# Optimization experiments

Measured on AMD Instinct MI355X. Metric: run time of the kernel, lower is better.

The kernel has to match this reference:

```python
import jax, jax.numpy as jnp
import numpy as np

B, T, N, E, H, MAXD = 32, 128, 42, 256, 8, 7
DH = E // H


def _hand_edges():
    left = [(0, 1), (1, 2), (2, 3), (3, 4), (0, 5), (5, 6), (6, 7), (7, 8), (0, 9), (9, 10), (10, 11), (11, 12), (0, 13), (13, 14), (14, 15), (15, 16), (0, 17), (17, 18), (18, 19), (19, 20)]
    right = [(21, 22), (22, 23), (23, 24), (24, 25), (21, 26), (26, 27), (27, 28), (28, 29), (21, 30), (30, 31), (31, 32), (32, 33), (21, 34), (34, 35), (35, 36), (36, 37), (21, 38), (38, 39), (39, 40), (40, 41)]
    tips = [(4, 8), (8, 12), (12, 16), (16, 20), (25, 29), (29, 33), (33, 37), (37, 41)]
    cross = [(0, 21)]
    return left + right + cross + tips


def _graph_constants():
    adj = np.zeros((N, N), dtype=np.float32)
    dist = np.zeros((N, N), dtype=np.float64)
    for a, b in _hand_edges():
        adj[a, b] = 1.0
        adj[b, a] = 1.0
        dist[a, b] = 1.0
        dist[b, a] = 1.0
    # exact replica of the module's single-pass Floyd-Warshall-style loop
    for k in range(N):
        for i in range(N):
            for j in range(N):
                if i != j and dist[i, k] > 0 and dist[k, j] > 0:
                    nd = dist[i, k] + dist[k, j]
                    if dist[i, j] == 0 or nd < dist[i, j]:
                        dist[i, j] = nd
    dist = np.clip(dist, 0, MAXD).astype(np.int32)
    return adj, dist


def setup_inputs() -> dict:
    key = jax.random.key(0)
    ks = jax.random.split(key, 12)
    adj_np, dist_np = _graph_constants()
    s_in = 1.0 / np.sqrt(E)
    return {
        'node_features': jax.random.normal(ks[0], (B, T, N, E), dtype=jnp.float32),
        'adjacency_matrix': jnp.asarray(adj_np),
        'distances': jnp.asarray(dist_np),
        'Wq': jax.random.normal(ks[1], (E, E), dtype=jnp.float32) * s_in,
        'bq': jnp.zeros((E,), dtype=jnp.float32),
        'Wk': jax.random.normal(ks[2], (E, E), dtype=jnp.float32) * s_in,
        'bk': jnp.zeros((E,), dtype=jnp.float32),
        'Wv': jax.random.normal(ks[3], (E, E), dtype=jnp.float32) * s_in,
        'bv': jnp.zeros((E,), dtype=jnp.float32),
        'Wo': jax.random.normal(ks[4], (E, E), dtype=jnp.float32) * s_in,
        'bo': jnp.zeros((E,), dtype=jnp.float32),
        'rel_emb': jax.random.normal(ks[5], (2 * MAXD + 1, H), dtype=jnp.float32) * 0.05,
    }


def reference(node_features, adjacency_matrix, distances, Wq, bq, Wk, bk, Wv, bv, Wo, bo, rel_emb):
    b, t, n, e = node_features.shape
    q = (node_features @ Wq + bq).reshape(b, t, n, H, DH)
    k = (node_features @ Wk + bk).reshape(b, t, n, H, DH)
    v = (node_features @ Wv + bv).reshape(b, t, n, H, DH)
    # scores: [b, t, h, i, j]
    scores = jnp.einsum('btihd,btjhd->bthij', q, k) / jnp.sqrt(jnp.float32(DH))
    # relative position bias: [n, n, h] -> [h, n, n]
    bias = rel_emb[distances]  # (N, N, H)
    scores = scores + jnp.transpose(bias, (2, 0, 1))[None, None]
    mask = (adjacency_matrix > 0).astype(jnp.float32)[None, None, None]
    scores = scores * mask + (1.0 - mask) * (-1e9)
    attn = jax.nn.softmax(scores, axis=-1)
    out = jnp.einsum('bthij,btjhd->btihd', attn, v).reshape(b, t, n, e)
    out = out @ Wo + bo
    return out, attn
```

## Files before the change

### kernel.cpp

```cpp
#include <hip/hip_runtime.h>
#include <stdint.h>


#define TPB 512
constexpr int BT = 4096;
constexpr int N = 42, NP = 48, E = 256, H = 8;
constexpr int NE = N * E;
constexpr int NN = N * N;
constexpr float SCALE = 0.17677669529663687f;

typedef short sh8 __attribute__((ext_vector_type(8)));
typedef float f4 __attribute__((ext_vector_type(4)));

__device__ __forceinline__ uint32_t cvtpk(float lo, float hi) {
  uint32_t d;
  asm("v_cvt_pk_bf16_f32 %0, %1, %2" : "=v"(d) : "v"(lo), "v"(hi));
  return d;
}
__device__ __forceinline__ uint16_t f2b1(float f) { return (uint16_t)cvtpk(f, f); }
__device__ __forceinline__ float b2f(uint16_t u) {
  union { uint32_t i; float f; } v; v.i = ((uint32_t)u) << 16; return v.f;
}

#define SWZ(base, row, cb) \
  ((char*)(base) + ((((row) << 9) + (cb)) ^ (((row) & 7) << 4)))

__global__ __launch_bounds__(256) void wt_kernel(
    const float* __restrict__ Wq, const float* __restrict__ Wk,
    const float* __restrict__ Wv, const float* __restrict__ Wo,
    uint16_t* __restrict__ WT) {
  __shared__ float tl[32][33];
  const int z = blockIdx.z;
  const float* W = (z == 0) ? Wq : (z == 1) ? Wk : (z == 2) ? Wv : Wo;
  uint16_t* dst = WT + z * 65536;
  const int k0 = blockIdx.y * 32, n0 = blockIdx.x * 32;
  const int r = threadIdx.x >> 5, cc = threadIdx.x & 31;
#pragma unroll
  for (int p = 0; p < 4; ++p)
    tl[r + 8 * p][cc] = W[(k0 + r + 8 * p) * E + n0 + cc];
  __syncthreads();
#pragma unroll
  for (int p = 0; p < 4; ++p)
    dst[(n0 + r + 8 * p) * E + k0 + cc] = f2b1(tl[cc][r + 8 * p]);
}

__device__ __forceinline__ void gemm_pass(const uint16_t* __restrict__ Wt,
                                          const char* Xb, int c, int lg, int nt0,
                                          f4 acc[3][2]) {
#pragma unroll
  for (int mt = 0; mt < 3; ++mt)
#pragma unroll
    for (int nt = 0; nt < 2; ++nt) acc[mt][nt] = (f4){0.f, 0.f, 0.f, 0.f};
  for (int kc = 0; kc < E; kc += 32) {
    sh8 xa[3];
#pragma unroll
    for (int mt = 0; mt < 3; ++mt)
      xa[mt] = *(const sh8*)SWZ(Xb, 16 * mt + c, (kc + 8 * lg) * 2);
#pragma unroll
    for (int nt = 0; nt < 2; ++nt) {
      const sh8 b8 = *(const sh8*)(Wt + ((nt0 + nt) * 16 + c) * E + kc + 8 * lg);
#pragma unroll
      for (int mt = 0; mt < 3; ++mt)
        acc[mt][nt] = __builtin_amdgcn_mfma_f32_16x16x32_bf16(xa[mt], b8, acc[mt][nt], 0, 0, 0);
    }
  }
}

__device__ __forceinline__ void tr_qk(const f4 acc[3][2], const float* __restrict__ bias,
                                      int n0, int c, int lg, uint16_t* scr, sh8 fr[3]) {
#pragma unroll
  for (int nt = 0; nt < 2; ++nt) {
    const float bv = bias[n0 + 16 * nt + c];
#pragma unroll
    for (int mt = 0; mt < 3; ++mt)
#pragma unroll
      for (int r = 0; r < 4; ++r)
        scr[(16 * mt + 4 * lg + r) * 40 + 16 * nt + c] = f2b1(acc[mt][nt][r] + bv);
  }
#pragma unroll
  for (int mt = 0; mt < 3; ++mt)
    fr[mt] = *(const sh8*)(scr + (16 * mt + c) * 40 + 8 * lg);
}

__global__ __launch_bounds__(TPB, 2) void gt_kernel(
    const float* __restrict__ X, const float* __restrict__ adj,
    const int* __restrict__ dist,
    const float* __restrict__ bq, const float* __restrict__ bk,
    const float* __restrict__ bv, const float* __restrict__ bo,
    const float* __restrict__ rel, const uint16_t* __restrict__ WT,
    float* __restrict__ out, float* __restrict__ attn) {
  alignas(16) __shared__ char smem[70368];
  char* const Xb = smem;
  uint16_t* const VT = (uint16_t*)smem;
  uint8_t*  const dm8 = (uint8_t*)(smem + 67584);
  float*    const relL = (float*)(smem + 69888);

  const int gid = blockIdx.x;
  const int tid = threadIdx.x;
  const int w = tid >> 6, lane = tid & 63, c = lane & 15, lg = lane >> 4;
  const int nt0 = 2 * w, n0 = 32 * w;
  uint16_t* const scr = (uint16_t*)(smem + 24576 + w * 5376);

  {
    const float4* Xs = (const float4*)(X + (size_t)gid * NE);
    for (int i = tid; i < NE / 4; i += TPB) {
      const float4 v = Xs[i];
      uint2 pk; pk.x = cvtpk(v.x, v.y); pk.y = cvtpk(v.z, v.w);
      *(uint2*)SWZ(Xb, i >> 6, (i & 63) << 3) = pk;
    }
    for (int i = tid; i < (NP - N) * 64; i += TPB) {
      uint2 z; z.x = 0u; z.y = 0u;
      *(uint2*)SWZ(Xb, N + (i >> 6), (i & 63) << 3) = z;
    }
    for (int t = tid; t < NP * NP; t += TPB) {
      const int i = t / NP, j = t - i * NP;
      uint8_t v = 0;
      if (i < N && j < N) {
        const float a = adj[i * N + j];
        v = (uint8_t)dist[i * N + j] | (a > 0.f ? 0x80 : 0);
      }
      dm8[t] = v;
    }
    for (int t = tid; t < 120; t += TPB) relL[t] = rel[t];
  }
  __syncthreads();

  sh8 qa[3], kb[3];
  {
    f4 acc[3][2];
    gemm_pass(WT, Xb, c, lg, nt0, acc);
    tr_qk(acc, bq, n0, c, lg, scr, qa);
    gemm_pass(WT + 65536, Xb, c, lg, nt0, acc);
    tr_qk(acc, bk, n0, c, lg, scr, kb);
  }
  f4 av[3][2];
  gemm_pass(WT + 131072, Xb, c, lg, nt0, av);
  __syncthreads();

#pragma unroll
  for (int nt = 0; nt < 2; ++nt) {
    const int n = n0 + 16 * nt + c;
    const float bvv = bv[n];
#pragma unroll
    for (int mt = 0; mt < 3; ++mt) {
      uint2 pk;
      pk.x = cvtpk(av[mt][nt][0] + bvv, av[mt][nt][1] + bvv);
      pk.y = cvtpk(av[mt][nt][2] + bvv, av[mt][nt][3] + bvv);
      *(uint2*)((char*)VT + n * 96 + 32 * mt + 8 * lg) = pk;
    }
  }

  {
    const int h = w;
    f4 st[3][3];
#pragma unroll
    for (int mt = 0; mt < 3; ++mt)
#pragma unroll
      for (int nt = 0; nt < 3; ++nt) {
        st[mt][nt] = (f4){0.f, 0.f, 0.f, 0.f};
        st[mt][nt] = __builtin_amdgcn_mfma_f32_16x16x32_bf16(kb[mt], qa[nt], st[mt][nt], 0, 0, 0);
      }

    uint16_t* const Psw = scr;
#pragma unroll
    for (int nt = 0; nt < 3; ++nt) {
      const int i = 16 * nt + c;
      float sv[12];
#pragma unroll
      for (int mt = 0; mt < 3; ++mt)
#pragma unroll
        for (int r = 0; r < 4; ++r) {
          const int j = 16 * mt + 4 * lg + r;
          const uint8_t dm = dm8[i * NP + j];
          const float s = st[mt][nt][r] * SCALE + relL[(dm & 0x7f) * 8 + h];
          sv[mt * 4 + r] = (dm & 0x80) ? s : -1e9f;
        }
      float m = sv[0];
#pragma unroll
      for (int k = 1; k < 12; ++k) m = fmaxf(m, sv[k]);
      m = fmaxf(m, __shfl_xor(m, 16));
      m = fmaxf(m, __shfl_xor(m, 32));
      float p[12], sum = 0.f;
#pragma unroll
      for (int k = 0; k < 12; ++k) { p[k] = __expf(sv[k] - m); sum += p[k]; }
      sum += __shfl_xor(sum, 16);
      sum += __shfl_xor(sum, 32);
      const float inv = __builtin_amdgcn_rcpf(sum);
#pragma unroll
      for (int mt = 0; mt < 3; ++mt) {
        const uint32_t d0 = cvtpk(p[mt * 4 + 0] * inv, p[mt * 4 + 1] * inv);
        const uint32_t d1 = cvtpk(p[mt * 4 + 2] * inv, p[mt * 4 + 3] * inv);
        char* base = (char*)Psw + i * 112 + 32 * mt + 8 * lg;
        *(uint32_t*)base = d0;
        *(uint32_t*)(base + 4) = d1;
      }
    }

    const sh8 z8 = {0, 0, 0, 0, 0, 0, 0, 0};
    sh8 pa0[3], pa1[3], vb0[2], vb1[2];
#pragma unroll
    for (int mt = 0; mt < 3; ++mt) {
      char* base = (char*)Psw + (16 * mt + c) * 112;
      pa0[mt] = *(const sh8*)(base + 16 * lg);
      pa1[mt] = (lg < 2) ? *(const sh8*)(base + 64 + 16 * lg) : z8;
    }
#pragma unroll
    for (int nt = 0; nt < 2; ++nt) {
      char* base = (char*)VT + (n0 + 16 * nt + c) * 96;
      vb0[nt] = *(const sh8*)(base + 16 * lg);
      vb1[nt] = (lg < 2) ? *(const sh8*)(base + 64 + 16 * lg) : z8;
    }
    f4 ov[3][2];
#pragma unroll
    for (int mt = 0; mt < 3; ++mt)
#pragma unroll
      for (int nt = 0; nt < 2; ++nt) {
        ov[mt][nt] = (f4){0.f, 0.f, 0.f, 0.f};
        ov[mt][nt] = __builtin_amdgcn_mfma_f32_16x16x32_bf16(pa0[mt], vb0[nt], ov[mt][nt], 0, 0, 0);
        ov[mt][nt] = __builtin_amdgcn_mfma_f32_16x16x32_bf16(pa1[mt], vb1[nt], ov[mt][nt], 0, 0, 0);
      }

    const size_t abase = ((size_t)gid * H + h) * (size_t)NN;
    for (int p = lane; p < NN; p += 64) {
      const int i = p / N, j = p - i * N;
      attn[abase + p] = b2f(Psw[i * 56 + j]);
    }
    __syncthreads();

#pragma unroll
    for (int mt = 0; mt < 3; ++mt)
#pragma unroll
      for (int nt = 0; nt < 2; ++nt)
#pragma unroll
        for (int r = 0; r < 4; ++r)
          *(uint16_t*)SWZ(Xb, 16 * mt + 4 * lg + r, (n0 + 16 * nt + c) * 2) =
              f2b1(ov[mt][nt][r]);
  }
  __syncthreads();

  {
    f4 ao[3][2];
    gemm_pass(WT + 196608, Xb, c, lg, nt0, ao);
#pragma unroll
    for (int nt = 0; nt < 2; ++nt) {
      const int n = n0 + 16 * nt + c;
      const float bov = bo[n];
#pragma unroll
      for (int mt = 0; mt < 3; ++mt)
#pragma unroll
        for (int r = 0; r < 4; ++r) {
          const int i = 16 * mt + 4 * lg + r;
          if (i < N) out[(size_t)gid * NE + i * E + n] = ao[mt][nt][r] + bov;
        }
    }
  }
}

extern "C" void kernel_launch(void* const* d_in, const int* in_sizes, int n_in,
                              void* d_out, int out_size, void* d_ws, size_t ws_size,
                              hipStream_t stream) {
  const float* X    = (const float*)d_in[0];
  const float* adj  = (const float*)d_in[1];
  const int*   dist = (const int*)d_in[2];
  const float* Wq   = (const float*)d_in[3];
  const float* bq   = (const float*)d_in[4];
  const float* Wk   = (const float*)d_in[5];
  const float* bk   = (const float*)d_in[6];
  const float* Wv   = (const float*)d_in[7];
  const float* bv   = (const float*)d_in[8];
  const float* Wo   = (const float*)d_in[9];
  const float* bo   = (const float*)d_in[10];
  const float* rel  = (const float*)d_in[11];
  float* out  = (float*)d_out;
  float* attn = out + (size_t)BT * NE;
  uint16_t* WT = (uint16_t*)d_ws;

  wt_kernel<<<dim3(8, 8, 4), dim3(256), 0, stream>>>(Wq, Wk, Wv, Wo, WT);
  gt_kernel<<<dim3(BT), dim3(TPB), 0, stream>>>(
      X, adj, dist, bq, bk, bv, bo, rel, WT, out, attn);
}
```

Before: 437.7 us.

## Split fused kernel into QKV projection and attention+output kernels via global scratch

Splits the single fused graph-transformer kernel into a QKV projection kernel and an attention plus Wo kernel. Q, K and transposed V are staged through workspace memory in bf16. The distance/adjacency byte table is precomputed once in the weight-transpose kernel. The aim is higher occupancy per kernel (launch bounds raised to 4 blocks) and shorter per-kernel register and LDS live ranges, at the cost of roughly 75 MB of extra global write and read traffic plus an extra launch.

```diff
diff --git a/kernel.cpp b/kernel.cpp
--- a/kernel.cpp
+++ b/kernel.cpp
@@ -9,6 +9,12 @@
 constexpr int NN = N * N;
 constexpr float SCALE = 0.17677669529663687f;
 
+constexpr size_t WT_OFF = 0;
+constexpr size_t DM_OFF = 524288;
+constexpr size_t Q_OFF  = 528384;
+constexpr size_t K_OFF  = Q_OFF + (size_t)BT * 48 * 256 * 2;
+constexpr size_t VT_OFF = K_OFF + (size_t)BT * 48 * 256 * 2;
+
 typedef short sh8 __attribute__((ext_vector_type(8)));
 typedef float f4 __attribute__((ext_vector_type(4)));
 
@@ -28,9 +34,22 @@
 __global__ __launch_bounds__(256) void wt_kernel(
     const float* __restrict__ Wq, const float* __restrict__ Wk,
     const float* __restrict__ Wv, const float* __restrict__ Wo,
-    uint16_t* __restrict__ WT) {
+    const float* __restrict__ adj, const int* __restrict__ dist,
+    uint16_t* __restrict__ WT, uint8_t* __restrict__ dm8g) {
+  const int z = blockIdx.z;
+  if (z == 4) {
+    if (blockIdx.x == 0 && blockIdx.y == 0) {
+      for (int t = threadIdx.x; t < NP * NP; t += 256) {
+        const int i = t / NP, j = t - i * NP;
+        uint8_t v = 0;
+        if (i < N && j < N)
+          v = (uint8_t)dist[i * N + j] | (adj[i * N + j] > 0.f ? 0x80 : 0);
+        dm8g[t] = v;
+      }
+    }
+    return;
+  }
   __shared__ float tl[32][33];
-  const int z = blockIdx.z;
   const float* W = (z == 0) ? Wq : (z == 1) ? Wk : (z == 2) ? Wv : Wo;
   uint16_t* dst = WT + z * 65536;
   const int k0 = blockIdx.y * 32, n0 = blockIdx.x * 32;
@@ -66,40 +85,17 @@
   }
 }
 
-__device__ __forceinline__ void tr_qk(const f4 acc[3][2], const float* __restrict__ bias,
-                                      int n0, int c, int lg, uint16_t* scr, sh8 fr[3]) {
-#pragma unroll
-  for (int nt = 0; nt < 2; ++nt) {
-    const float bv = bias[n0 + 16 * nt + c];
-#pragma unroll
-    for (int mt = 0; mt < 3; ++mt)
-#pragma unroll
-      for (int r = 0; r < 4; ++r)
-        scr[(16 * mt + 4 * lg + r) * 40 + 16 * nt + c] = f2b1(acc[mt][nt][r] + bv);
-  }
-#pragma unroll
-  for (int mt = 0; mt < 3; ++mt)
-    fr[mt] = *(const sh8*)(scr + (16 * mt + c) * 40 + 8 * lg);
-}
-
-__global__ __launch_bounds__(TPB, 2) void gt_kernel(
-    const float* __restrict__ X, const float* __restrict__ adj,
-    const int* __restrict__ dist,
+__global__ __launch_bounds__(TPB, 4) void qkv_kernel(
+    const float* __restrict__ X,
     const float* __restrict__ bq, const float* __restrict__ bk,
-    const float* __restrict__ bv, const float* __restrict__ bo,
-    const float* __restrict__ rel, const uint16_t* __restrict__ WT,
-    float* __restrict__ out, float* __restrict__ attn) {
-  alignas(16) __shared__ char smem[70368];
-  char* const Xb = smem;
-  uint16_t* const VT = (uint16_t*)smem;
-  uint8_t*  const dm8 = (uint8_t*)(smem + 67584);
-  float*    const relL = (float*)(smem + 69888);
-
+    const float* __restrict__ bv, const uint16_t* __restrict__ WT,
+    uint16_t* __restrict__ Qg, uint16_t* __restrict__ Kg,
+    char* __restrict__ VTg) {
+  alignas(16) __shared__ char Xb[NP * 512];
   const int gid = blockIdx.x;
   const int tid = threadIdx.x;
   const int w = tid >> 6, lane = tid & 63, c = lane & 15, lg = lane >> 4;
   const int nt0 = 2 * w, n0 = 32 * w;
-  uint16_t* const scr = (uint16_t*)(smem + 24576 + w * 5376);
 
   {
     const float4* Xs = (const float4*)(X + (size_t)gid * NE);
@@ -112,135 +108,170 @@
       uint2 z; z.x = 0u; z.y = 0u;
       *(uint2*)SWZ(Xb, N + (i >> 6), (i & 63) << 3) = z;
     }
-    for (int t = tid; t < NP * NP; t += TPB) {
-      const int i = t / NP, j = t - i * NP;
-      uint8_t v = 0;
-      if (i < N && j < N) {
-        const float a = adj[i * N + j];
-        v = (uint8_t)dist[i * N + j] | (a > 0.f ? 0x80 : 0);
-      }
-      dm8[t] = v;
-    }
-    for (int t = tid; t < 120; t += TPB) relL[t] = rel[t];
   }
   __syncthreads();
 
-  sh8 qa[3], kb[3];
-  {
-    f4 acc[3][2];
-    gemm_pass(WT, Xb, c, lg, nt0, acc);
-    tr_qk(acc, bq, n0, c, lg, scr, qa);
-    gemm_pass(WT + 65536, Xb, c, lg, nt0, acc);
-    tr_qk(acc, bk, n0, c, lg, scr, kb);
-  }
-  f4 av[3][2];
-  gemm_pass(WT + 131072, Xb, c, lg, nt0, av);
-  __syncthreads();
-
+  f4 acc[3][2];
+  gemm_pass(WT, Xb, c, lg, nt0, acc);
 #pragma unroll
   for (int nt = 0; nt < 2; ++nt) {
     const int n = n0 + 16 * nt + c;
-    const float bvv = bv[n];
+    const float bv_ = bq[n];
+#pragma unroll
+    for (int mt = 0; mt < 3; ++mt)
+#pragma unroll
+      for (int r = 0; r < 4; ++r) {
+        const int i = 16 * mt + 4 * lg + r;
+        Qg[((size_t)gid * 48 + i) * 256 + n] = f2b1(acc[mt][nt][r] + bv_);
+      }
+  }
+  gemm_pass(WT + 65536, Xb, c, lg, nt0, acc);
+#pragma unroll
+  for (int nt = 0; nt < 2; ++nt) {
+    const int n = n0 + 16 * nt + c;
+    const float bv_ = bk[n];
+#pragma unroll
+    for (int mt = 0; mt < 3; ++mt)
+#pragma unroll
+      for (int r = 0; r < 4; ++r) {
+        const int i = 16 * mt + 4 * lg + r;
+        Kg[((size_t)gid * 48 + i) * 256 + n] = f2b1(acc[mt][nt][r] + bv_);
+      }
+  }
+  gemm_pass(WT + 131072, Xb, c, lg, nt0, acc);
+  char* const vt = VTg + (size_t)gid * 24576;
+#pragma unroll
+  for (int nt = 0; nt < 2; ++nt) {
+    const int n = n0 + 16 * nt + c;
+    const float bv_ = bv[n];
 #pragma unroll
     for (int mt = 0; mt < 3; ++mt) {
       uint2 pk;
-      pk.x = cvtpk(av[mt][nt][0] + bvv, av[mt][nt][1] + bvv);
-      pk.y = cvtpk(av[mt][nt][2] + bvv, av[mt][nt][3] + bvv);
-      *(uint2*)((char*)VT + n * 96 + 32 * mt + 8 * lg) = pk;
+      pk.x = cvtpk(acc[mt][nt][0] + bv_, acc[mt][nt][1] + bv_);
+      pk.y = cvtpk(acc[mt][nt][2] + bv_, acc[mt][nt][3] + bv_);
+      *(uint2*)(vt + n * 96 + 32 * mt + 8 * lg) = pk;
+    }
+  }
+}
+
+__global__ __launch_bounds__(TPB, 4) void attn_wo_kernel(
+    const float* __restrict__ bo, const float* __restrict__ rel,
+    const uint16_t* __restrict__ WT, const uint16_t* __restrict__ Qg,
+    const uint16_t* __restrict__ Kg, const char* __restrict__ VTg,
+    const uint8_t* __restrict__ dm8g,
+    float* __restrict__ out, float* __restrict__ attn) {
+  alignas(16) __shared__ char smem[70368];
+  char* const Ob = smem;
+  uint8_t* const dm8 = (uint8_t*)(smem + 67584);
+  float*   const relL = (float*)(smem + 69888);
+
+  const int gid = blockIdx.x;
+  const int tid = threadIdx.x;
+  const int w = tid >> 6, lane = tid & 63, c = lane & 15, lg = lane >> 4;
+  const int nt0 = 2 * w, n0 = 32 * w, h = w;
+  uint16_t* const scr = (uint16_t*)(smem + 24576 + w * 5376);
+
+  for (int t = tid; t < NP * NP; t += TPB) dm8[t] = dm8g[t];
+  for (int t = tid; t < 120; t += TPB) relL[t] = rel[t];
+  __syncthreads();
+
+  sh8 qa[3], kb[3];
+#pragma unroll
+  for (int mt = 0; mt < 3; ++mt) {
+    const size_t ro = ((size_t)gid * 48 + 16 * mt + c) * 256 + 32 * h + 8 * lg;
+    qa[mt] = *(const sh8*)(Qg + ro);
+    kb[mt] = *(const sh8*)(Kg + ro);
+  }
+
+  f4 st[3][3];
+#pragma unroll
+  for (int mt = 0; mt < 3; ++mt)
+#pragma unroll
+    for (int nt = 0; nt < 3; ++nt) {
+      st[mt][nt] = (f4){0.f, 0.f, 0.f, 0.f};
+      st[mt][nt] = __builtin_amdgcn_mfma_f32_16x16x32_bf16(kb[mt], qa[nt], st[mt][nt], 0, 0, 0);
+    }
+
+  uint16_t* const Psw = scr;
+#pragma unroll
+  for (int nt = 0; nt < 3; ++nt) {
+    const int i = 16 * nt + c;
+    float sv[12];
+#pragma unroll
+    for (int mt = 0; mt < 3; ++mt)
+#pragma unroll
+      for (int r = 0; r < 4; ++r) {
+        const int j = 16 * mt + 4 * lg + r;
+        const uint8_t dm = dm8[i * NP + j];
+        const float s = st[mt][nt][r] * SCALE + relL[(dm & 0x7f) * 8 + h];
+        sv[mt * 4 + r] = (dm & 0x80) ? s : -1e9f;
+      }
+    float m = sv[0];
+#pragma unroll
+    for (int k = 1; k < 12; ++k) m = fmaxf(m, sv[k]);
+    m = fmaxf(m, __shfl_xor(m, 16));
+    m = fmaxf(m, __shfl_xor(m, 32));
+    float p[12], sum = 0.f;
+#pragma unroll
+    for (int k = 0; k < 12; ++k) { p[k] = __expf(sv[k] - m); sum += p[k]; }
+    sum += __shfl_xor(sum, 16);
+    sum += __shfl_xor(sum, 32);
+    const float inv = __builtin_amdgcn_rcpf(sum);
+#pragma unroll
+    for (int mt = 0; mt < 3; ++mt) {
+      const uint32_t d0 = cvtpk(p[mt * 4 + 0] * inv, p[mt * 4 + 1] * inv);
+      const uint32_t d1 = cvtpk(p[mt * 4 + 2] * inv, p[mt * 4 + 3] * inv);
+      char* base = (char*)Psw + i * 112 + 32 * mt + 8 * lg;
+      *(uint32_t*)base = d0;
+      *(uint32_t*)(base + 4) = d1;
     }
   }
 
   {
-    const int h = w;
-    f4 st[3][3];
-#pragma unroll
-    for (int mt = 0; mt < 3; ++mt)
-#pragma unroll
-      for (int nt = 0; nt < 3; ++nt) {
-        st[mt][nt] = (f4){0.f, 0.f, 0.f, 0.f};
-        st[mt][nt] = __builtin_amdgcn_mfma_f32_16x16x32_bf16(kb[mt], qa[nt], st[mt][nt], 0, 0, 0);
-      }
-
-    uint16_t* const Psw = scr;
-#pragma unroll
-    for (int nt = 0; nt < 3; ++nt) {
-      const int i = 16 * nt + c;
-      float sv[12];
-#pragma unroll
-      for (int mt = 0; mt < 3; ++mt)
-#pragma unroll
-        for (int r = 0; r < 4; ++r) {
-          const int j = 16 * mt + 4 * lg + r;
-          const uint8_t dm = dm8[i * NP + j];
-          const float s = st[mt][nt][r] * SCALE + relL[(dm & 0x7f) * 8 + h];
-          sv[mt * 4 + r] = (dm & 0x80) ? s : -1e9f;
-        }
-      float m = sv[0];
-#pragma unroll
-      for (int k = 1; k < 12; ++k) m = fmaxf(m, sv[k]);
-      m = fmaxf(m, __shfl_xor(m, 16));
-      m = fmaxf(m, __shfl_xor(m, 32));
-      float p[12], sum = 0.f;
-#pragma unroll
-      for (int k = 0; k < 12; ++k) { p[k] = __expf(sv[k] - m); sum += p[k]; }
-      sum += __shfl_xor(sum, 16);
-      sum += __shfl_xor(sum, 32);
-      const float inv = __builtin_amdgcn_rcpf(sum);
-#pragma unroll
-      for (int mt = 0; mt < 3; ++mt) {
-        const uint32_t d0 = cvtpk(p[mt * 4 + 0] * inv, p[mt * 4 + 1] * inv);
-        const uint32_t d1 = cvtpk(p[mt * 4 + 2] * inv, p[mt * 4 + 3] * inv);
-        char* base = (char*)Psw + i * 112 + 32 * mt + 8 * lg;
-        *(uint32_t*)base = d0;
-        *(uint32_t*)(base + 4) = d1;
-      }
-    }
-
-    const sh8 z8 = {0, 0, 0, 0, 0, 0, 0, 0};
-    sh8 pa0[3], pa1[3], vb0[2], vb1[2];
-#pragma unroll
-    for (int mt = 0; mt < 3; ++mt) {
-      char* base = (char*)Psw + (16 * mt + c) * 112;
-      pa0[mt] = *(const sh8*)(base + 16 * lg);
-      pa1[mt] = (lg < 2) ? *(const sh8*)(base + 64 + 16 * lg) : z8;
-    }
-#pragma unroll
-    for (int nt = 0; nt < 2; ++nt) {
-      char* base = (char*)VT + (n0 + 16 * nt + c) * 96;
-      vb0[nt] = *(const sh8*)(base + 16 * lg);
-      vb1[nt] = (lg < 2) ? *(const sh8*)(base + 64 + 16 * lg) : z8;
-    }
-    f4 ov[3][2];
-#pragma unroll
-    for (int mt = 0; mt < 3; ++mt)
-#pragma unroll
-      for (int nt = 0; nt < 2; ++nt) {
-        ov[mt][nt] = (f4){0.f, 0.f, 0.f, 0.f};
-        ov[mt][nt] = __builtin_amdgcn_mfma_f32_16x16x32_bf16(pa0[mt], vb0[nt], ov[mt][nt], 0, 0, 0);
-        ov[mt][nt] = __builtin_amdgcn_mfma_f32_16x16x32_bf16(pa1[mt], vb1[nt], ov[mt][nt], 0, 0, 0);
-      }
-
     const size_t abase = ((size_t)gid * H + h) * (size_t)NN;
     for (int p = lane; p < NN; p += 64) {
       const int i = p / N, j = p - i * N;
       attn[abase + p] = b2f(Psw[i * 56 + j]);
     }
-    __syncthreads();
-
-#pragma unroll
-    for (int mt = 0; mt < 3; ++mt)
-#pragma unroll
-      for (int nt = 0; nt < 2; ++nt)
-#pragma unroll
-        for (int r = 0; r < 4; ++r)
-          *(uint16_t*)SWZ(Xb, 16 * mt + 4 * lg + r, (n0 + 16 * nt + c) * 2) =
-              f2b1(ov[mt][nt][r]);
-  }
+  }
+
+  const sh8 z8 = {0, 0, 0, 0, 0, 0, 0, 0};
+  sh8 pa0[3], pa1[3], vb0[2], vb1[2];
+#pragma unroll
+  for (int mt = 0; mt < 3; ++mt) {
+    char* base = (char*)Psw + (16 * mt + c) * 112;
+    pa0[mt] = *(const sh8*)(base + 16 * lg);
+    pa1[mt] = (lg < 2) ? *(const sh8*)(base + 64 + 16 * lg) : z8;
+  }
+#pragma unroll
+  for (int nt = 0; nt < 2; ++nt) {
+    const char* base = VTg + (size_t)gid * 24576 + (h * 32 + 16 * nt + c) * 96;
+    vb0[nt] = *(const sh8*)(base + 16 * lg);
+    vb1[nt] = (lg < 2) ? *(const sh8*)(base + 64 + 16 * lg) : z8;
+  }
+  f4 ov[3][2];
+#pragma unroll
+  for (int mt = 0; mt < 3; ++mt)
+#pragma unroll
+    for (int nt = 0; nt < 2; ++nt) {
+      ov[mt][nt] = (f4){0.f, 0.f, 0.f, 0.f};
+      ov[mt][nt] = __builtin_amdgcn_mfma_f32_16x16x32_bf16(pa0[mt], vb0[nt], ov[mt][nt], 0, 0, 0);
+      ov[mt][nt] = __builtin_amdgcn_mfma_f32_16x16x32_bf16(pa1[mt], vb1[nt], ov[mt][nt], 0, 0, 0);
+    }
+
+#pragma unroll
+  for (int mt = 0; mt < 3; ++mt)
+#pragma unroll
+    for (int nt = 0; nt < 2; ++nt)
+#pragma unroll
+      for (int r = 0; r < 4; ++r)
+        *(uint16_t*)SWZ(Ob, 16 * mt + 4 * lg + r, (n0 + 16 * nt + c) * 2) =
+            f2b1(ov[mt][nt][r]);
   __syncthreads();
 
   {
     f4 ao[3][2];
-    gemm_pass(WT + 196608, Xb, c, lg, nt0, ao);
+    gemm_pass(WT + 196608, Ob, c, lg, nt0, ao);
 #pragma unroll
     for (int nt = 0; nt < 2; ++nt) {
       const int n = n0 + 16 * nt + c;
@@ -273,9 +304,15 @@
   const float* rel  = (const float*)d_in[11];
   float* out  = (float*)d_out;
   float* attn = out + (size_t)BT * NE;
-  uint16_t* WT = (uint16_t*)d_ws;
-
-  wt_kernel<<<dim3(8, 8, 4), dim3(256), 0, stream>>>(Wq, Wk, Wv, Wo, WT);
-  gt_kernel<<<dim3(BT), dim3(TPB), 0, stream>>>(
-      X, adj, dist, bq, bk, bv, bo, rel, WT, out, attn);
-}
+
+  char* ws = (char*)d_ws;
+  uint16_t* WT   = (uint16_t*)(ws + WT_OFF);
+  uint8_t*  dm8g = (uint8_t*)(ws + DM_OFF);
+  uint16_t* Qg   = (uint16_t*)(ws + Q_OFF);
+  uint16_t* Kg   = (uint16_t*)(ws + K_OFF);
+  char*     VTg  = ws + VT_OFF;
+
+  wt_kernel<<<dim3(8, 8, 5), dim3(256), 0, stream>>>(Wq, Wk, Wv, Wo, adj, dist, WT, dm8g);
+  qkv_kernel<<<dim3(BT), dim3(TPB), 0, stream>>>(X, bq, bk, bv, WT, Qg, Kg, VTg);
+  attn_wo_kernel<<<dim3(BT), dim3(TPB), 0, stream>>>(bo, rel, WT, Qg, Kg, VTg, dm8g, out, attn);
+}
```

Result: slower. 457.5 us (+4.5%).
